# Optimization experiments

Measured on AMD Instinct MI355X. Metric: run time of the kernel, lower is better.

## Reference

```python
import jax, jax.numpy as jnp
import numpy as np
from jax import lax


def setup_inputs() -> dict:
    key = jax.random.key(0)
    ks = jax.random.split(key, 7)
    B, S, D, E = 4, 4096, 1024, 8
    H = 4 * D
    scale = 0.02
    x = jax.random.normal(ks[0], (B, S, D), dtype=jnp.float32)
    Wg = jax.random.normal(ks[1], (D, E), dtype=jnp.float32) * scale
    bg = jnp.zeros((E,), dtype=jnp.float32)
    W1 = jax.random.normal(ks[2], (E, D, H), dtype=jnp.float32) * scale
    b1 = jnp.zeros((E, H), dtype=jnp.float32)
    W2 = jax.random.normal(ks[3], (E, H, D), dtype=jnp.float32) * scale
    b2 = jnp.zeros((E, D), dtype=jnp.float32)
    return {"x": x, "Wg": Wg, "bg": bg, "W1": W1, "b1": b1,
            "W2": W2, "b2": b2, "topk_num": 2}


def _moe_forward(x, Wg, bg, W1, b1, W2, b2, topk_num):
    B, S, D = x.shape
    E = Wg.shape[1]
    flat_x = x.reshape(-1, D)                      # (T, D)
    T = flat_x.shape[0]
    # Router: clean logits (source bug: noise computed on noisy_logits but
    # topk/softmax operate on `logits`), sparse softmax over top-k experts.
    logits = flat_x @ Wg + bg                      # (T, E)
    topk_vals, topk_idx = lax.top_k(logits, topk_num)   # (T, k)
    probs = jax.nn.softmax(topk_vals, axis=-1)     # softmax over -inf-masked == softmax over topk
    gates = jnp.zeros((T, E), dtype=x.dtype).at[
        jnp.arange(T)[:, None], topk_idx].set(probs)    # (T, E), 0 for unrouted
    # Dispatch/compute/combine: gate weight is exactly 0 for unrouted tokens,
    # so a dense per-expert FFN weighted by the gate matches the masked
    # gather-FFN-scatter math of the original.
    out = jnp.zeros_like(flat_x)
    for e in range(E):
        h = jax.nn.relu(flat_x @ W1[e] + b1[e])    # (T, 4D)
        y = h @ W2[e] + b2[e]                      # (T, D)
        out = out + gates[:, e:e + 1] * y
    return out.reshape(B, S, D)


def reference(x, Wg, bg, W1, b1, W2, b2, topk_num):
    return _moe_forward(x, Wg, bg, W1, b1, W2, b2, topk_num)
```

## Files before the change

### kernel.cpp

```cpp
#include <hip/hip_runtime.h>
#include <cstdint>
#include <cstddef>

typedef unsigned short u16;
typedef __bf16 bf16x8 __attribute__((ext_vector_type(8)));
typedef u16    u16x8  __attribute__((ext_vector_type(8)));
typedef float  f32x4  __attribute__((ext_vector_type(4)));

static __device__ __forceinline__ u16 f2bf(float f) {
  uint32_t u = __builtin_bit_cast(uint32_t, f);
  u += 0x7FFFu + ((u >> 16) & 1u);
  return (u16)(u >> 16);
}
static __device__ __forceinline__ float bf2f(u16 h) {
  return __builtin_bit_cast(float, (uint32_t)h << 16);
}
static __device__ __forceinline__ bf16x8 as_bf(u16x8 v) {
  union { u16x8 u; bf16x8 b; } x; x.u = v; return x.b;
}

#define GLD_LDS(src, dst)                                                      \
  __builtin_amdgcn_global_load_lds(                                            \
      (const __attribute__((address_space(1))) void*)(const void*)(src),       \
      (__attribute__((address_space(3))) void*)(void*)(dst), 16, 0, 0)

#define T_TOK 16384
#define DDIM  1024
#define EEXP  8
#define HDIM  4096
#define BM256 256
#define MAXTILES 136
#define MAXSLOTS 34816

__global__ __launch_bounds__(256) void transpose_cast64(
    const float* __restrict__ in, u16* __restrict__ out, int R, int C) {
  __shared__ float t[64][65];
  int e = blockIdx.z;
  const float* src = in + (size_t)e * R * C;
  u16* dst = out + (size_t)e * R * C;
  int r0 = blockIdx.y << 6, c0 = blockIdx.x << 6;
  int tr = threadIdx.x >> 4;
  int tc = (threadIdx.x & 15) << 2;
#pragma unroll
  for (int i = 0; i < 4; i++) {
    const float4 v = *(const float4*)(src + (size_t)(r0 + tr + i * 16) * C + c0 + tc);
    t[tr + i * 16][tc + 0] = v.x;
    t[tr + i * 16][tc + 1] = v.y;
    t[tr + i * 16][tc + 2] = v.z;
    t[tr + i * 16][tc + 3] = v.w;
  }
  __syncthreads();
  int oc = threadIdx.x >> 3;
  int rr = (threadIdx.x & 7) << 3;
#pragma unroll
  for (int i = 0; i < 2; i++) {
    int c = oc + (i << 5);
    u16x8 o;
#pragma unroll
    for (int j = 0; j < 8; j++) o[j] = f2bf(t[rr + j][c]);
    *(u16x8*)(dst + (size_t)(c0 + c) * R + r0 + rr) = o;
  }
}

__global__ __launch_bounds__(256) void router_kernel(
    const float* __restrict__ x, const float* __restrict__ Wg,
    const float* __restrict__ bg, u16* __restrict__ xbf,
    int2* __restrict__ tok_e, float2* __restrict__ tok_g,
    int* __restrict__ counts) {
  int w = threadIdx.x >> 6, lane = threadIdx.x & 63;
  int t = blockIdx.x * 4 + w;
  const float* xr = x + (size_t)t * DDIM;
  float acc[EEXP] = {0.f, 0.f, 0.f, 0.f, 0.f, 0.f, 0.f, 0.f};
#pragma unroll
  for (int j = 0; j < DDIM / 64; j++) {
    int d = j * 64 + lane;
    float xv = xr[d];
    xbf[(size_t)t * DDIM + d] = f2bf(xv);
    const float4* wv = (const float4*)(Wg + (size_t)d * EEXP);
    float4 wa = wv[0], wb = wv[1];
    acc[0] += xv * wa.x; acc[1] += xv * wa.y;
    acc[2] += xv * wa.z; acc[3] += xv * wa.w;
    acc[4] += xv * wb.x; acc[5] += xv * wb.y;
    acc[6] += xv * wb.z; acc[7] += xv * wb.w;
  }
#pragma unroll
  for (int e = 0; e < EEXP; e++) {
    float v = acc[e];
    for (int s = 32; s; s >>= 1) v += __shfl_xor(v, s);
    acc[e] = v + bg[e];
  }
  int e0 = 0; float v0 = acc[0];
#pragma unroll
  for (int e = 1; e < EEXP; e++) if (acc[e] > v0) { v0 = acc[e]; e0 = e; }
  int e1 = -1; float v1 = -3.402823466e38f;
#pragma unroll
  for (int e = 0; e < EEXP; e++)
    if (e != e0 && acc[e] > v1) { v1 = acc[e]; e1 = e; }
  float p0 = 1.f / (1.f + expf(v1 - v0));
  float p1 = 1.f - p0;
  if (lane == 0) {
    atomicAdd(&counts[e0], 1);
    atomicAdd(&counts[e1], 1);
    tok_e[t] = make_int2(e0, e1);
    tok_g[t] = make_float2(p0, p1);
  }
}

__global__ void scan_kernel(const int* __restrict__ counts,
                            int* __restrict__ expBase,
                            int* __restrict__ tileExpert,
                            int* __restrict__ tileRow0,
                            int* __restrict__ nTiles) {
  if (threadIdx.x != 0 || blockIdx.x != 0) return;
  int base = 0, nt = 0;
  for (int e = 0; e < EEXP; e++) {
    expBase[e] = base;
    int c = counts[e];
    int tiles = (c + BM256 - 1) >> 8;
    for (int i = 0; i < tiles; i++) {
      tileExpert[nt] = e;
      tileRow0[nt] = base + (i << 8);
      nt++;
    }
    base += tiles << 8;
  }
  *nTiles = nt;
}

__global__ __launch_bounds__(256) void scatter_kernel(
    const int2* __restrict__ tok_e, int* __restrict__ cursor,
    const int* __restrict__ expBase, int* __restrict__ rowmap,
    float* __restrict__ gateOf, const float2* __restrict__ tok_g) {
  int t = blockIdx.x * 256 + threadIdx.x;
  int2 e = tok_e[t];
  float2 g = tok_g[t];
  int s0 = expBase[e.x] + atomicAdd(&cursor[e.x], 1);
  int s1 = expBase[e.y] + atomicAdd(&cursor[e.y], 1);
  rowmap[s0] = t;
  rowmap[s1] = t;
  gateOf[s0] = g.x;
  gateOf[s1] = g.y;
}

template <bool RELU_STORE, bool GATHER, bool ATOMIC_OUT>
__global__ __launch_bounds__(512) void moe_gemm256(
    const u16* __restrict__ A,
    const u16* __restrict__ Bt,
    const float* __restrict__ bias,
    u16* __restrict__ Cbf,
    float* __restrict__ Cout,
    const float* __restrict__ gateOf, const int* __restrict__ rowmap,
    const int* __restrict__ tileExpert, const int* __restrict__ tileRow0,
    const int* __restrict__ nTiles, int N, int K) {
  __shared__ __align__(16) u16 As[2][256 * 64];
  __shared__ __align__(16) u16 Bs[2][256 * 64];
  int ntl = N >> 8;
  int nwg = (int)gridDim.x;
  int bid = (int)blockIdx.x;
  int swzb = (bid & 7) * (nwg >> 3) + (bid >> 3);
  int mtile = swzb / ntl, ntile = swzb - mtile * ntl;
  if (mtile >= *nTiles) return;
  int e = tileExpert[mtile];
  int row0 = tileRow0[mtile];
  int ncol0 = ntile << 8;
  const u16* Bm = Bt + (size_t)e * N * K;
  const float* bb = bias + (size_t)e * N;

  int tid = threadIdx.x;
  int wv = tid >> 6, lane = tid & 63;
  int wr = wv >> 2, wc = wv & 3;
  int rlo = lane & 15, hi = lane >> 4;

  int srow = tid >> 3;
  int gkc = (tid & 7) ^ (srow & 7);
  const u16* asrc[4]; const u16* bsrc[4];
#pragma unroll
  for (int j = 0; j < 4; j++) {
    int row = j * 64 + srow;
    int ar = GATHER ? rowmap[row0 + row] : (row0 + row);
    asrc[j] = A + (size_t)ar * K + gkc * 8;
    bsrc[j] = Bm + (size_t)(ncol0 + row) * K + gkc * 8;
  }

  f32x4 acc[8][4] = {};
  int nkt = K >> 6;

#pragma unroll
  for (int j = 0; j < 4; j++) GLD_LDS(asrc[j], &As[0][j * 4096 + wv * 512]);
#pragma unroll
  for (int j = 0; j < 4; j++) GLD_LDS(bsrc[j], &Bs[0][j * 4096 + wv * 512]);

  int swA0 = ((hi + 0) ^ (rlo & 7)) * 8;
  int swA4 = ((hi + 4) ^ (rlo & 7)) * 8;

  for (int kt = 0; kt < nkt; ++kt) {
    const u16* as = As[kt & 1];
    const u16* bs = Bs[kt & 1];
    u16* an = As[(kt & 1) ^ 1];
    u16* bn = Bs[(kt & 1) ^ 1];
    int sk = (kt + 1) << 6;
    bool pf = (kt + 1 < nkt);

    asm volatile("s_waitcnt vmcnt(0)" ::: "memory");
    __builtin_amdgcn_s_barrier();
    __builtin_amdgcn_sched_barrier(0);

    u16x8 af[4][2], b0[2][2], b1[2][2];
    if (pf) {
#pragma unroll
      for (int j = 0; j < 4; j++) GLD_LDS(asrc[j] + sk, &an[j * 4096 + wv * 512]);
    }
#pragma unroll
    for (int m = 0; m < 4; m++) {
      int rb = (wr * 128 + m * 16 + rlo) * 64;
      af[m][0] = *(const u16x8*)(as + rb + swA0);
      af[m][1] = *(const u16x8*)(as + rb + swA4);
    }
#pragma unroll
    for (int n = 0; n < 2; n++) {
      int rb = (wc * 64 + n * 16 + rlo) * 64;
      b0[n][0] = *(const u16x8*)(bs + rb + swA0);
      b0[n][1] = *(const u16x8*)(bs + rb + swA4);
    }
    __builtin_amdgcn_s_setprio(1);
#pragma unroll
    for (int m = 0; m < 4; m++)
#pragma unroll
      for (int n = 0; n < 2; n++) {
        acc[m][n] = __builtin_amdgcn_mfma_f32_16x16x32_bf16(as_bf(af[m][0]), as_bf(b0[n][0]), acc[m][n], 0, 0, 0);
        acc[m][n] = __builtin_amdgcn_mfma_f32_16x16x32_bf16(as_bf(af[m][1]), as_bf(b0[n][1]), acc[m][n], 0, 0, 0);
      }
    __builtin_amdgcn_s_setprio(0);
    __builtin_amdgcn_s_barrier();

    if (pf) {
#pragma unroll
      for (int j = 0; j < 4; j++) GLD_LDS(bsrc[j] + sk, &bn[j * 4096 + wv * 512]);
    }
#pragma unroll
    for (int n = 0; n < 2; n++) {
      int rb = (wc * 64 + (n + 2) * 16 + rlo) * 64;
      b1[n][0] = *(const u16x8*)(bs + rb + swA0);
      b1[n][1] = *(const u16x8*)(bs + rb + swA4);
    }
    __builtin_amdgcn_s_setprio(1);
#pragma unroll
    for (int m = 0; m < 4; m++)
#pragma unroll
      for (int n = 0; n < 2; n++) {
        acc[m][n + 2] = __builtin_amdgcn_mfma_f32_16x16x32_bf16(as_bf(af[m][0]), as_bf(b1[n][0]), acc[m][n + 2], 0, 0, 0);
        acc[m][n + 2] = __builtin_amdgcn_mfma_f32_16x16x32_bf16(as_bf(af[m][1]), as_bf(b1[n][1]), acc[m][n + 2], 0, 0, 0);
      }
    __builtin_amdgcn_s_setprio(0);
    __builtin_amdgcn_s_barrier();

#pragma unroll
    for (int m = 0; m < 4; m++) {
      int rb = (wr * 128 + (m + 4) * 16 + rlo) * 64;
      af[m][0] = *(const u16x8*)(as + rb + swA0);
      af[m][1] = *(const u16x8*)(as + rb + swA4);
    }
    __builtin_amdgcn_s_setprio(1);
#pragma unroll
    for (int m = 0; m < 4; m++)
#pragma unroll
      for (int n = 0; n < 2; n++) {
        acc[m + 4][n + 2] = __builtin_amdgcn_mfma_f32_16x16x32_bf16(as_bf(af[m][0]), as_bf(b1[n][0]), acc[m + 4][n + 2], 0, 0, 0);
        acc[m + 4][n + 2] = __builtin_amdgcn_mfma_f32_16x16x32_bf16(as_bf(af[m][1]), as_bf(b1[n][1]), acc[m + 4][n + 2], 0, 0, 0);
      }
    __builtin_amdgcn_s_setprio(0);
    __builtin_amdgcn_s_barrier();

    __builtin_amdgcn_s_setprio(1);
#pragma unroll
    for (int m = 0; m < 4; m++)
#pragma unroll
      for (int n = 0; n < 2; n++) {
        acc[m + 4][n] = __builtin_amdgcn_mfma_f32_16x16x32_bf16(as_bf(af[m][0]), as_bf(b0[n][0]), acc[m + 4][n], 0, 0, 0);
        acc[m + 4][n] = __builtin_amdgcn_mfma_f32_16x16x32_bf16(as_bf(af[m][1]), as_bf(b0[n][1]), acc[m + 4][n], 0, 0, 0);
      }
    __builtin_amdgcn_s_setprio(0);
  }

  asm volatile("s_waitcnt vmcnt(0)" ::: "memory");
  int r4 = hi * 4;
  if (!ATOMIC_OUT) {
#pragma unroll
    for (int m = 0; m < 8; m++) {
      int rb = row0 + wr * 128 + m * 16 + r4;
#pragma unroll
      for (int n = 0; n < 4; n++) {
        int col = ncol0 + wc * 64 + n * 16 + rlo;
        float bv = bb[col];
#pragma unroll
        for (int j = 0; j < 4; j++) {
          float v = acc[m][n][j] + bv;
          if (RELU_STORE) v = fmaxf(v, 0.f);
          Cbf[(size_t)(rb + j) * N + col] = f2bf(v);
        }
      }
    }
  } else {
#pragma unroll
    for (int m = 0; m < 8; m++) {
      int rb = row0 + wr * 128 + m * 16 + r4;
#pragma unroll
      for (int j = 0; j < 4; j++) {
        int slot = rb + j;
        float g = gateOf[slot];
        if (g != 0.f) {
          int t = rowmap[slot];
          float* op = Cout + (size_t)t * DDIM;
#pragma unroll
          for (int n = 0; n < 4; n++) {
            int col = ncol0 + wc * 64 + n * 16 + rlo;
            atomicAdd(op + col, g * (acc[m][n][j] + bb[col]));
          }
        }
      }
    }
  }
}

extern "C" void kernel_launch(void* const* d_in, const int* in_sizes, int n_in,
                              void* d_out, int out_size, void* d_ws,
                              size_t ws_size, hipStream_t stream) {
  (void)in_sizes; (void)n_in; (void)ws_size;
  const float* x  = (const float*)d_in[0];
  const float* Wg = (const float*)d_in[1];
  const float* bg = (const float*)d_in[2];
  const float* W1 = (const float*)d_in[3];
  const float* b1 = (const float*)d_in[4];
  const float* W2 = (const float*)d_in[5];
  const float* b2 = (const float*)d_in[6];
  float* out = (float*)d_out;

  char* ws = (char*)d_ws;
  size_t o = 0;
  u16* W1T = (u16*)(ws + o); o += (size_t)EEXP * DDIM * HDIM * 2;
  u16* W2T = (u16*)(ws + o); o += (size_t)EEXP * HDIM * DDIM * 2;
  u16* xbf = (u16*)(ws + o); o += (size_t)T_TOK * DDIM * 2;
  u16* Hbuf = (u16*)(ws + o); o += (size_t)MAXSLOTS * HDIM * 2;
  int* rowmap = (int*)(ws + o); o += (size_t)MAXSLOTS * 4;
  float* gateOf = (float*)(ws + o); o += (size_t)MAXSLOTS * 4;
  int2* tok_e = (int2*)(ws + o); o += (size_t)T_TOK * 8;
  float2* tok_g = (float2*)(ws + o); o += (size_t)T_TOK * 8;
  int* counts = (int*)(ws + o); o += 8 * 4;
  int* cursor = (int*)(ws + o); o += 8 * 4;
  int* expBase = (int*)(ws + o); o += 8 * 4;
  int* nTiles = (int*)(ws + o); o += 8 * 4;
  int* tileExpert = (int*)(ws + o); o += MAXTILES * 4;
  int* tileRow0 = (int*)(ws + o); o += MAXTILES * 4;

  hipMemsetAsync(counts, 0, 16 * 4, stream);
  hipMemsetAsync(rowmap, 0, (size_t)MAXSLOTS * 4, stream);
  hipMemsetAsync(gateOf, 0, (size_t)MAXSLOTS * 4, stream);
  hipMemsetAsync(out, 0, (size_t)out_size * 4, stream);

  transpose_cast64<<<dim3(HDIM / 64, DDIM / 64, EEXP), 256, 0, stream>>>(W1, W1T, DDIM, HDIM);
  transpose_cast64<<<dim3(DDIM / 64, HDIM / 64, EEXP), 256, 0, stream>>>(W2, W2T, HDIM, DDIM);

  router_kernel<<<T_TOK / 4, 256, 0, stream>>>(x, Wg, bg, xbf, tok_e, tok_g, counts);
  scan_kernel<<<1, 64, 0, stream>>>(counts, expBase, tileExpert, tileRow0, nTiles);
  scatter_kernel<<<T_TOK / 256, 256, 0, stream>>>(tok_e, cursor, expBase, rowmap, gateOf, tok_g);

  moe_gemm256<true, true, false><<<MAXTILES * (HDIM / 256), 512, 0, stream>>>(
      xbf, W1T, b1, Hbuf, nullptr, nullptr, rowmap, tileExpert, tileRow0, nTiles, HDIM, DDIM);
  moe_gemm256<false, false, true><<<MAXTILES * (DDIM / 256), 512, 0, stream>>>(
      Hbuf, W2T, b2, nullptr, out, gateOf, rowmap, tileExpert, tileRow0, nTiles, DDIM, HDIM);
}
```

Measured before the change: 2.011 ms.

## Split GEMM tiles into half-tile stages and replace atomic combine with gather kernel

The grouped GEMM now stages A and B in 128-row halves with finer-grained vmcnt waits, so each half-tile load overlaps MFMA work on the other half instead of waiting for the whole tile every k-step. The second GEMM writes per-slot bf16 outputs to a buffer (reusing the xbf space), and a new combine kernel gathers each token's two expert outputs and applies the gates. This removes the float atomics and the output memset. In exchange it adds an extra pass over the intermediate output, and the output now goes through bf16 rounding before gating.

```diff
diff --git a/kernel.cpp b/kernel.cpp
--- a/kernel.cpp
+++ b/kernel.cpp
@@ -18,11 +18,22 @@
 static __device__ __forceinline__ bf16x8 as_bf(u16x8 v) {
   union { u16x8 u; bf16x8 b; } x; x.u = v; return x.b;
 }
+static __device__ __forceinline__ f32x4 mf(u16x8 a, u16x8 b, f32x4 c) {
+  return __builtin_amdgcn_mfma_f32_16x16x32_bf16(as_bf(a), as_bf(b), c, 0, 0, 0);
+}
 
 #define GLD_LDS(src, dst)                                                      \
   __builtin_amdgcn_global_load_lds(                                            \
       (const __attribute__((address_space(1))) void*)(const void*)(src),       \
       (__attribute__((address_space(3))) void*)(void*)(dst), 16, 0, 0)
+
+#define VMC6 asm volatile("s_waitcnt vmcnt(6)" ::: "memory")
+#define VMC4 asm volatile("s_waitcnt vmcnt(4)" ::: "memory")
+#define VMC2 asm volatile("s_waitcnt vmcnt(2)" ::: "memory")
+#define VMC0 asm volatile("s_waitcnt vmcnt(0)" ::: "memory")
+#define LGK0 do { asm volatile("s_waitcnt lgkmcnt(0)" ::: "memory"); \
+                  __builtin_amdgcn_sched_barrier(0); } while (0)
+#define BARR __builtin_amdgcn_s_barrier()
 
 #define T_TOK 16384
 #define DDIM  1024
@@ -130,33 +141,29 @@
 __global__ __launch_bounds__(256) void scatter_kernel(
     const int2* __restrict__ tok_e, int* __restrict__ cursor,
     const int* __restrict__ expBase, int* __restrict__ rowmap,
-    float* __restrict__ gateOf, const float2* __restrict__ tok_g) {
+    int2* __restrict__ tokslot) {
   int t = blockIdx.x * 256 + threadIdx.x;
   int2 e = tok_e[t];
-  float2 g = tok_g[t];
   int s0 = expBase[e.x] + atomicAdd(&cursor[e.x], 1);
   int s1 = expBase[e.y] + atomicAdd(&cursor[e.y], 1);
   rowmap[s0] = t;
   rowmap[s1] = t;
-  gateOf[s0] = g.x;
-  gateOf[s1] = g.y;
-}
-
-template <bool RELU_STORE, bool GATHER, bool ATOMIC_OUT>
-__global__ __launch_bounds__(512) void moe_gemm256(
+  tokslot[t] = make_int2(s0, s1);
+}
+
+template <bool RELU, bool GATHER>
+__global__ __launch_bounds__(512) void moe_gemm8p(
     const u16* __restrict__ A,
     const u16* __restrict__ Bt,
     const float* __restrict__ bias,
-    u16* __restrict__ Cbf,
-    float* __restrict__ Cout,
-    const float* __restrict__ gateOf, const int* __restrict__ rowmap,
+    u16* __restrict__ C,
+    const int* __restrict__ rowmap,
     const int* __restrict__ tileExpert, const int* __restrict__ tileRow0,
     const int* __restrict__ nTiles, int N, int K) {
-  __shared__ __align__(16) u16 As[2][256 * 64];
-  __shared__ __align__(16) u16 Bs[2][256 * 64];
+  __shared__ __align__(16) u16 As[2][2][128 * 64];
+  __shared__ __align__(16) u16 Bs[2][2][128 * 64];
   int ntl = N >> 8;
-  int nwg = (int)gridDim.x;
-  int bid = (int)blockIdx.x;
+  int nwg = (int)gridDim.x, bid = (int)blockIdx.x;
   int swzb = (bid & 7) * (nwg >> 3) + (bid >> 3);
   int mtile = swzb / ntl, ntile = swzb - mtile * ntl;
   if (mtile >= *nTiles) return;
@@ -166,166 +173,168 @@
   const u16* Bm = Bt + (size_t)e * N * K;
   const float* bb = bias + (size_t)e * N;
 
-  int tid = threadIdx.x;
-  int wv = tid >> 6, lane = tid & 63;
+  int tid = threadIdx.x, lane = tid & 63, wv = tid >> 6;
   int wr = wv >> 2, wc = wv & 3;
   int rlo = lane & 15, hi = lane >> 4;
 
-  int srow = tid >> 3;
-  int gkc = (tid & 7) ^ (srow & 7);
-  const u16* asrc[4]; const u16* bsrc[4];
-#pragma unroll
-  for (int j = 0; j < 4; j++) {
-    int row = j * 64 + srow;
-    int ar = GATHER ? rowmap[row0 + row] : (row0 + row);
-    asrc[j] = A + (size_t)ar * K + gkc * 8;
-    bsrc[j] = Bm + (size_t)(ncol0 + row) * K + gkc * 8;
-  }
+  int rr0 = tid >> 3;
+  int kc = (tid & 7) ^ (rr0 & 7);
+  const u16 *aS[2][2], *bS[2][2];
+#pragma unroll
+  for (int h = 0; h < 2; h++) {
+    int r0g = row0 + h * 128 + rr0, r1g = r0g + 64;
+    int ar0 = GATHER ? rowmap[r0g] : r0g;
+    int ar1 = GATHER ? rowmap[r1g] : r1g;
+    aS[h][0] = A + (size_t)ar0 * K + kc * 8;
+    aS[h][1] = A + (size_t)ar1 * K + kc * 8;
+    bS[h][0] = Bm + (size_t)(ncol0 + h * 128 + rr0) * K + kc * 8;
+    bS[h][1] = Bm + (size_t)(ncol0 + h * 128 + rr0 + 64) * K + kc * 8;
+  }
+  int d0 = tid * 8, d1 = d0 + 4096;
+
+#define ST_A(h_, buf_, k0_) do { \
+    GLD_LDS(aS[h_][0] + (k0_), &As[buf_][h_][d0]); \
+    GLD_LDS(aS[h_][1] + (k0_), &As[buf_][h_][d1]); } while (0)
+#define ST_B(h_, buf_, k0_) do { \
+    GLD_LDS(bS[h_][0] + (k0_), &Bs[buf_][h_][d0]); \
+    GLD_LDS(bS[h_][1] + (k0_), &Bs[buf_][h_][d1]); } while (0)
+
+  int sw0 = ((hi + 0) ^ (rlo & 7)) * 8;
+  int sw1 = ((hi + 4) ^ (rlo & 7)) * 8;
 
   f32x4 acc[8][4] = {};
+  u16x8 af[4][2], b0f[2][2], b1f[2][2];
   int nkt = K >> 6;
 
-#pragma unroll
-  for (int j = 0; j < 4; j++) GLD_LDS(asrc[j], &As[0][j * 4096 + wv * 512]);
-#pragma unroll
-  for (int j = 0; j < 4; j++) GLD_LDS(bsrc[j], &Bs[0][j * 4096 + wv * 512]);
-
-  int swA0 = ((hi + 0) ^ (rlo & 7)) * 8;
-  int swA4 = ((hi + 4) ^ (rlo & 7)) * 8;
-
-  for (int kt = 0; kt < nkt; ++kt) {
-    const u16* as = As[kt & 1];
-    const u16* bs = Bs[kt & 1];
-    u16* an = As[(kt & 1) ^ 1];
-    u16* bn = Bs[(kt & 1) ^ 1];
-    int sk = (kt + 1) << 6;
-    bool pf = (kt + 1 < nkt);
-
-    asm volatile("s_waitcnt vmcnt(0)" ::: "memory");
-    __builtin_amdgcn_s_barrier();
-    __builtin_amdgcn_sched_barrier(0);
-
-    u16x8 af[4][2], b0[2][2], b1[2][2];
-    if (pf) {
-#pragma unroll
-      for (int j = 0; j < 4; j++) GLD_LDS(asrc[j] + sk, &an[j * 4096 + wv * 512]);
-    }
+  ST_A(0, 0, 0); ST_B(0, 0, 0); ST_B(1, 0, 0); ST_A(1, 0, 0); ST_A(0, 1, 64);
+  VMC6; BARR;
+
+  for (int t = 0; t < nkt; ++t) {
+    int bc = t & 1, bn = bc ^ 1;
+    int sk = (t + 1) << 6;
+    const bool st1 = (t + 1 < nkt), st2 = (t + 2 < nkt);
+    const u16* Ac0 = &As[bc][0][0];
+    const u16* Ac1 = &As[bc][1][0];
+    const u16* Bc0 = &Bs[bc][0][0];
+    const u16* Bc1 = &Bs[bc][1][0];
+
 #pragma unroll
     for (int m = 0; m < 4; m++) {
-      int rb = (wr * 128 + m * 16 + rlo) * 64;
-      af[m][0] = *(const u16x8*)(as + rb + swA0);
-      af[m][1] = *(const u16x8*)(as + rb + swA4);
+      int ro = (wr * 64 + m * 16 + rlo) * 64;
+      af[m][0] = *(const u16x8*)(Ac0 + ro + sw0);
+      af[m][1] = *(const u16x8*)(Ac0 + ro + sw1);
     }
 #pragma unroll
     for (int n = 0; n < 2; n++) {
-      int rb = (wc * 64 + n * 16 + rlo) * 64;
-      b0[n][0] = *(const u16x8*)(bs + rb + swA0);
-      b0[n][1] = *(const u16x8*)(bs + rb + swA4);
-    }
+      int ro = (wc * 32 + n * 16 + rlo) * 64;
+      b0f[n][0] = *(const u16x8*)(Bc0 + ro + sw0);
+      b0f[n][1] = *(const u16x8*)(Bc0 + ro + sw1);
+    }
+    if (st1) { ST_B(0, bn, sk); VMC6; } else { VMC2; }
+    BARR; LGK0;
     __builtin_amdgcn_s_setprio(1);
 #pragma unroll
     for (int m = 0; m < 4; m++)
 #pragma unroll
       for (int n = 0; n < 2; n++) {
-        acc[m][n] = __builtin_amdgcn_mfma_f32_16x16x32_bf16(as_bf(af[m][0]), as_bf(b0[n][0]), acc[m][n], 0, 0, 0);
-        acc[m][n] = __builtin_amdgcn_mfma_f32_16x16x32_bf16(as_bf(af[m][1]), as_bf(b0[n][1]), acc[m][n], 0, 0, 0);
+        acc[m][n] = mf(af[m][0], b0f[n][0], acc[m][n]);
+        acc[m][n] = mf(af[m][1], b0f[n][1], acc[m][n]);
       }
     __builtin_amdgcn_s_setprio(0);
-    __builtin_amdgcn_s_barrier();
-
-    if (pf) {
-#pragma unroll
-      for (int j = 0; j < 4; j++) GLD_LDS(bsrc[j] + sk, &bn[j * 4096 + wv * 512]);
-    }
+    BARR;
+
 #pragma unroll
     for (int n = 0; n < 2; n++) {
-      int rb = (wc * 64 + (n + 2) * 16 + rlo) * 64;
-      b1[n][0] = *(const u16x8*)(bs + rb + swA0);
-      b1[n][1] = *(const u16x8*)(bs + rb + swA4);
-    }
+      int ro = (wc * 32 + n * 16 + rlo) * 64;
+      b1f[n][0] = *(const u16x8*)(Bc1 + ro + sw0);
+      b1f[n][1] = *(const u16x8*)(Bc1 + ro + sw1);
+    }
+    if (st1) { ST_B(1, bn, sk); VMC6; } else { VMC0; }
+    BARR; LGK0;
     __builtin_amdgcn_s_setprio(1);
 #pragma unroll
     for (int m = 0; m < 4; m++)
 #pragma unroll
       for (int n = 0; n < 2; n++) {
-        acc[m][n + 2] = __builtin_amdgcn_mfma_f32_16x16x32_bf16(as_bf(af[m][0]), as_bf(b1[n][0]), acc[m][n + 2], 0, 0, 0);
-        acc[m][n + 2] = __builtin_amdgcn_mfma_f32_16x16x32_bf16(as_bf(af[m][1]), as_bf(b1[n][1]), acc[m][n + 2], 0, 0, 0);
+        acc[m][n + 2] = mf(af[m][0], b1f[n][0], acc[m][n + 2]);
+        acc[m][n + 2] = mf(af[m][1], b1f[n][1], acc[m][n + 2]);
       }
     __builtin_amdgcn_s_setprio(0);
-    __builtin_amdgcn_s_barrier();
+    BARR;
 
 #pragma unroll
     for (int m = 0; m < 4; m++) {
-      int rb = (wr * 128 + (m + 4) * 16 + rlo) * 64;
-      af[m][0] = *(const u16x8*)(as + rb + swA0);
-      af[m][1] = *(const u16x8*)(as + rb + swA4);
-    }
+      int ro = (wr * 64 + m * 16 + rlo) * 64;
+      af[m][0] = *(const u16x8*)(Ac1 + ro + sw0);
+      af[m][1] = *(const u16x8*)(Ac1 + ro + sw1);
+    }
+    if (st1) { ST_A(1, bn, sk); VMC6; } else { VMC0; }
+    BARR; LGK0;
     __builtin_amdgcn_s_setprio(1);
 #pragma unroll
     for (int m = 0; m < 4; m++)
 #pragma unroll
       for (int n = 0; n < 2; n++) {
-        acc[m + 4][n + 2] = __builtin_amdgcn_mfma_f32_16x16x32_bf16(as_bf(af[m][0]), as_bf(b1[n][0]), acc[m + 4][n + 2], 0, 0, 0);
-        acc[m + 4][n + 2] = __builtin_amdgcn_mfma_f32_16x16x32_bf16(as_bf(af[m][1]), as_bf(b1[n][1]), acc[m + 4][n + 2], 0, 0, 0);
+        acc[m + 4][n + 2] = mf(af[m][0], b1f[n][0], acc[m + 4][n + 2]);
+        acc[m + 4][n + 2] = mf(af[m][1], b1f[n][1], acc[m + 4][n + 2]);
       }
     __builtin_amdgcn_s_setprio(0);
-    __builtin_amdgcn_s_barrier();
-
+    BARR;
+
+    if (st2) { ST_A(0, bc, sk + 64); VMC6; }
+    else if (st1) { VMC4; }
+    else { VMC0; }
+    BARR;
     __builtin_amdgcn_s_setprio(1);
 #pragma unroll
     for (int m = 0; m < 4; m++)
 #pragma unroll
       for (int n = 0; n < 2; n++) {
-        acc[m + 4][n] = __builtin_amdgcn_mfma_f32_16x16x32_bf16(as_bf(af[m][0]), as_bf(b0[n][0]), acc[m + 4][n], 0, 0, 0);
-        acc[m + 4][n] = __builtin_amdgcn_mfma_f32_16x16x32_bf16(as_bf(af[m][1]), as_bf(b0[n][1]), acc[m + 4][n], 0, 0, 0);
+        acc[m + 4][n] = mf(af[m][0], b0f[n][0], acc[m + 4][n]);
+        acc[m + 4][n] = mf(af[m][1], b0f[n][1], acc[m + 4][n]);
       }
     __builtin_amdgcn_s_setprio(0);
-  }
-
-  asm volatile("s_waitcnt vmcnt(0)" ::: "memory");
-  int r4 = hi * 4;
-  if (!ATOMIC_OUT) {
-#pragma unroll
-    for (int m = 0; m < 8; m++) {
-      int rb = row0 + wr * 128 + m * 16 + r4;
-#pragma unroll
-      for (int n = 0; n < 4; n++) {
-        int col = ncol0 + wc * 64 + n * 16 + rlo;
-        float bv = bb[col];
-#pragma unroll
-        for (int j = 0; j < 4; j++) {
-          float v = acc[m][n][j] + bv;
-          if (RELU_STORE) v = fmaxf(v, 0.f);
-          Cbf[(size_t)(rb + j) * N + col] = f2bf(v);
-        }
-      }
-    }
-  } else {
-#pragma unroll
-    for (int m = 0; m < 8; m++) {
-      int rb = row0 + wr * 128 + m * 16 + r4;
+    BARR;
+  }
+
+#pragma unroll
+  for (int rf = 0; rf < 8; rf++) {
+    int rb = row0 + (rf >> 2) * 128 + wr * 64 + (rf & 3) * 16 + hi * 4;
+#pragma unroll
+    for (int cf = 0; cf < 4; cf++) {
+      int col = ncol0 + (cf >> 1) * 128 + wc * 32 + (cf & 1) * 16 + rlo;
+      float bv = bb[col];
 #pragma unroll
       for (int j = 0; j < 4; j++) {
-        int slot = rb + j;
-        float g = gateOf[slot];
-        if (g != 0.f) {
-          int t = rowmap[slot];
-          float* op = Cout + (size_t)t * DDIM;
-#pragma unroll
-          for (int n = 0; n < 4; n++) {
-            int col = ncol0 + wc * 64 + n * 16 + rlo;
-            atomicAdd(op + col, g * (acc[m][n][j] + bb[col]));
-          }
-        }
-      }
-    }
-  }
+        float v = acc[rf][cf][j] + bv;
+        if (RELU) v = fmaxf(v, 0.f);
+        C[(size_t)(rb + j) * N + col] = f2bf(v);
+      }
+    }
+  }
+#undef ST_A
+#undef ST_B
+}
+
+__global__ __launch_bounds__(256) void combine_kernel(
+    const u16* __restrict__ Y, const int2* __restrict__ tokslot,
+    const float2* __restrict__ tok_g, float* __restrict__ out) {
+  int gid = blockIdx.x * 256 + threadIdx.x;
+  int t = gid >> 7, seg = (gid & 127) * 8;
+  int2 s = tokslot[t];
+  float2 g = tok_g[t];
+  u16x8 y0 = *reinterpret_cast<const u16x8*>(Y + (size_t)s.x * DDIM + seg);
+  u16x8 y1 = *reinterpret_cast<const u16x8*>(Y + (size_t)s.y * DDIM + seg);
+  float* op = out + (size_t)t * DDIM + seg;
+#pragma unroll
+  for (int i = 0; i < 8; i++)
+    op[i] = g.x * bf2f(y0[i]) + g.y * bf2f(y1[i]);
 }
 
 extern "C" void kernel_launch(void* const* d_in, const int* in_sizes, int n_in,
                               void* d_out, int out_size, void* d_ws,
                               size_t ws_size, hipStream_t stream) {
-  (void)in_sizes; (void)n_in; (void)ws_size;
+  (void)in_sizes; (void)n_in; (void)out_size; (void)ws_size;
   const float* x  = (const float*)d_in[0];
   const float* Wg = (const float*)d_in[1];
   const float* bg = (const float*)d_in[2];
@@ -337,35 +346,36 @@
 
   char* ws = (char*)d_ws;
   size_t o = 0;
-  u16* W1T = (u16*)(ws + o); o += (size_t)EEXP * DDIM * HDIM * 2;
-  u16* W2T = (u16*)(ws + o); o += (size_t)EEXP * HDIM * DDIM * 2;
-  u16* xbf = (u16*)(ws + o); o += (size_t)T_TOK * DDIM * 2;
+  u16* W2T  = (u16*)(ws + o); o += (size_t)EEXP * HDIM * DDIM * 2;
   u16* Hbuf = (u16*)(ws + o); o += (size_t)MAXSLOTS * HDIM * 2;
+  u16* xbf  = (u16*)(ws + o); o += (size_t)T_TOK * DDIM * 2;
+  u16* W1T  = (u16*)(ws + o); o += (size_t)EEXP * DDIM * HDIM * 2;
   int* rowmap = (int*)(ws + o); o += (size_t)MAXSLOTS * 4;
-  float* gateOf = (float*)(ws + o); o += (size_t)MAXSLOTS * 4;
   int2* tok_e = (int2*)(ws + o); o += (size_t)T_TOK * 8;
   float2* tok_g = (float2*)(ws + o); o += (size_t)T_TOK * 8;
+  int2* tokslot = (int2*)(ws + o); o += (size_t)T_TOK * 8;
   int* counts = (int*)(ws + o); o += 8 * 4;
   int* cursor = (int*)(ws + o); o += 8 * 4;
   int* expBase = (int*)(ws + o); o += 8 * 4;
   int* nTiles = (int*)(ws + o); o += 8 * 4;
   int* tileExpert = (int*)(ws + o); o += MAXTILES * 4;
   int* tileRow0 = (int*)(ws + o); o += MAXTILES * 4;
+  u16* Ybuf = xbf;
 
   hipMemsetAsync(counts, 0, 16 * 4, stream);
   hipMemsetAsync(rowmap, 0, (size_t)MAXSLOTS * 4, stream);
-  hipMemsetAsync(gateOf, 0, (size_t)MAXSLOTS * 4, stream);
-  hipMemsetAsync(out, 0, (size_t)out_size * 4, stream);
 
   transpose_cast64<<<dim3(HDIM / 64, DDIM / 64, EEXP), 256, 0, stream>>>(W1, W1T, DDIM, HDIM);
   transpose_cast64<<<dim3(DDIM / 64, HDIM / 64, EEXP), 256, 0, stream>>>(W2, W2T, HDIM, DDIM);
 
   router_kernel<<<T_TOK / 4, 256, 0, stream>>>(x, Wg, bg, xbf, tok_e, tok_g, counts);
   scan_kernel<<<1, 64, 0, stream>>>(counts, expBase, tileExpert, tileRow0, nTiles);
-  scatter_kernel<<<T_TOK / 256, 256, 0, stream>>>(tok_e, cursor, expBase, rowmap, gateOf, tok_g);
-
-  moe_gemm256<true, true, false><<<MAXTILES * (HDIM / 256), 512, 0, stream>>>(
-      xbf, W1T, b1, Hbuf, nullptr, nullptr, rowmap, tileExpert, tileRow0, nTiles, HDIM, DDIM);
-  moe_gemm256<false, false, true><<<MAXTILES * (DDIM / 256), 512, 0, stream>>>(
-      Hbuf, W2T, b2, nullptr, out, gateOf, rowmap, tileExpert, tileRow0, nTiles, DDIM, HDIM);
-}
+  scatter_kernel<<<T_TOK / 256, 256, 0, stream>>>(tok_e, cursor, expBase, rowmap, tokslot);
+
+  moe_gemm8p<true, true><<<MAXTILES * (HDIM / 256), 512, 0, stream>>>(
+      xbf, W1T, b1, Hbuf, rowmap, tileExpert, tileRow0, nTiles, HDIM, DDIM);
+  moe_gemm8p<false, false><<<MAXTILES * (DDIM / 256), 512, 0, stream>>>(
+      Hbuf, W2T, b2, Ybuf, nullptr, tileExpert, tileRow0, nTiles, DDIM, HDIM);
+
+  combine_kernel<<<(T_TOK * (DDIM / 8)) / 256, 256, 0, stream>>>(Ybuf, tokslot, tok_g, out);
+}
```

Result: faster. 1.656 ms (-17.6%).
